# Kernel tuning notes

Measured on AMD Instinct MI355X. Metric: run time of the kernel, lower is better.

Reference implementation:

```python
import jax, jax.numpy as jnp
import numpy as np

B, H, W = 16, 512, 512


def conv2d(x, w, b):
    # NCHW conv, stride 1, padding 1 (SAME for 3x3)
    y = jax.lax.conv_general_dilated(
        x, w, window_strides=(1, 1), padding=((1, 1), (1, 1)),
        dimension_numbers=("NCHW", "OIHW", "NCHW"))
    return y + b[None, :, None, None]


def bilinear_sample(img, py, px):
    # img: [B,H,W]; py,px: [B,K,H,W] float sample coords. Zero padding outside.
    Hh, Ww = img.shape[1], img.shape[2]
    y0 = jnp.floor(py)
    x0 = jnp.floor(px)
    wy = py - y0  # fractional weights
    wx = px - x0
    y0i = y0.astype(jnp.int32)
    x0i = x0.astype(jnp.int32)

    def gather(yi, xi):
        valid = (yi >= 0) & (yi < Hh) & (xi >= 0) & (xi < Ww)
        yc = jnp.clip(yi, 0, Hh - 1)
        xc = jnp.clip(xi, 0, Ww - 1)
        v = jax.vmap(lambda im, yy, xx: im[yy, xx])(img, yc, xc)
        return jnp.where(valid, v, jnp.zeros((), img.dtype))

    v00 = gather(y0i, x0i)
    v01 = gather(y0i, x0i + 1)
    v10 = gather(y0i + 1, x0i)
    v11 = gather(y0i + 1, x0i + 1)
    return (v00 * (1 - wy) * (1 - wx) + v01 * (1 - wy) * wx
            + v10 * wy * (1 - wx) + v11 * wy * wx)


def setup_inputs() -> dict:
    key = jax.random.key(0)
    ks = jax.random.split(key, 7)
    pm25 = jax.random.normal(ks[0], (B, 1, H, W), jnp.float32)
    avg_wind = jax.random.normal(ks[1], (B, 2, H, W), jnp.float32)
    topo = jax.random.normal(ks[2], (B, 1, H, W), jnp.float32)
    # offset_conv params (Kaiming-ish small random)
    conv1_w = jax.random.normal(ks[3], (16, 3, 3, 3), jnp.float32) * (1.0 / np.sqrt(3 * 9))
    conv1_b = jax.random.normal(ks[4], (16,), jnp.float32) * 0.01
    conv2_w = jax.random.normal(ks[5], (18, 16, 3, 3), jnp.float32) * (1.0 / np.sqrt(16 * 9))
    conv2_b = jax.random.normal(ks[6], (18,), jnp.float32) * 0.01
    # dirac init: identity 3x3 kernel
    weight = jnp.zeros((1, 1, 3, 3), jnp.float32).at[0, 0, 1, 1].set(1.0)
    return {"pm25": pm25, "avg_wind": avg_wind, "topo": topo,
            "conv1_w": conv1_w, "conv1_b": conv1_b,
            "conv2_w": conv2_w, "conv2_b": conv2_b, "weight": weight}


def reference(pm25, avg_wind, topo, conv1_w, conv1_b, conv2_w, conv2_b, weight):
    # offset-predicting conv stack
    feat = jax.nn.gelu(conv2d(jnp.concatenate([avg_wind, topo], axis=1), conv1_w, conv1_b), approximate=False)
    offsets = conv2d(feat, conv2_w, conv2_b)          # [B, 2*3*3, H, W]
    b, _, h, w = offsets.shape
    off = offsets.reshape(b, 9, 2, h, w)              # k = i*3 + j; [.,k,0]=dy, [.,k,1]=dx
    dy, dx = off[:, :, 0], off[:, :, 1]               # [B,9,H,W]

    ys = jnp.arange(h, dtype=pm25.dtype)[None, None, :, None]
    xs = jnp.arange(w, dtype=pm25.dtype)[None, None, None, :]
    ki = jnp.arange(3, dtype=pm25.dtype)
    kdy = (jnp.repeat(ki, 3) - 1.0)[None, :, None, None]  # kernel row offset - pad
    kdx = (jnp.tile(ki, 3) - 1.0)[None, :, None, None]    # kernel col offset - pad

    py = ys + kdy + dy                                # sample rows   [B,9,H,W]
    px = xs + kdx + dx                                # sample cols   [B,9,H,W]

    samp = bilinear_sample(pm25[:, 0], py, px)        # [B,9,H,W]
    wk = weight.reshape(9)                            # single-channel 3x3 kernel
    out = jnp.einsum("bkhw,k->bhw", samp, wk)[:, None]
    return out                                        # [B,1,H,W]
```

## Files before the change

kernel.cpp:

```cpp
#include <hip/hip_runtime.h>
#include <math.h>

#define Bn 16
#define Hh 512
#define Ww 512
#define HW_ (Hh * Ww)
#define TILE 32
#define NTHREADS 1024
#define S 37
#define SIN_N 1400
#define NFP 1280
#define NT2 80

typedef __bf16 bfrag __attribute__((ext_vector_type(8)));
typedef __bf16 bf4   __attribute__((ext_vector_type(4)));
typedef float  ffrag __attribute__((ext_vector_type(16)));
typedef float  f32x4 __attribute__((ext_vector_type(4)));
typedef float  f32x2 __attribute__((ext_vector_type(2)));

__device__ __forceinline__ short f2bf(float f) {
    unsigned u = __float_as_uint(f);
    unsigned r = u + 0x7FFFu + ((u >> 16) & 1u);
    return (short)(r >> 16);
}

__device__ __forceinline__ f32x2 mk2(float a, float b) { f32x2 t; t.x = a; t.y = b; return t; }

__device__ __forceinline__ f32x2 gelu_fast2(f32x2 x) {
    f32x2 z = x * x;
    f32x2 a = z * 0.044715f + 1.0f;
    f32x2 u = (x * 2.302208199f) * a;
    f32x2 e;
    e.x = __builtin_amdgcn_exp2f(u.x);
    e.y = __builtin_amdgcn_exp2f(u.y);
    f32x2 r;
    r.x = __builtin_amdgcn_rcpf(e.x + 1.0f);
    r.y = __builtin_amdgcn_rcpf(e.y + 1.0f);
    return x - x * r;
}

__device__ __forceinline__ float bilin(const float* __restrict__ img, float py, float px) {
    float y0f = floorf(py), x0f = floorf(px);
    float wy = py - y0f, wx = px - x0f;
    int y0 = (int)y0f, x0 = (int)x0f;
    int yc0 = min(max(y0, 0), Hh - 1), yc1 = min(max(y0 + 1, 0), Hh - 1);
    int xc0 = min(max(x0, 0), Ww - 1), xc1 = min(max(x0 + 1, 0), Ww - 1);
    bool vy0 = (unsigned)y0 < (unsigned)Hh, vy1 = (unsigned)(y0 + 1) < (unsigned)Hh;
    bool vx0 = (unsigned)x0 < (unsigned)Ww, vx1 = (unsigned)(x0 + 1) < (unsigned)Ww;
    const float* r0 = img + yc0 * Ww;
    const float* r1 = img + yc1 * Ww;
    float v00 = (vy0 && vx0) ? r0[xc0] : 0.0f;
    float v01 = (vy0 && vx1) ? r0[xc1] : 0.0f;
    float v10 = (vy1 && vx0) ? r1[xc0] : 0.0f;
    float v11 = (vy1 && vx1) ? r1[xc1] : 0.0f;
    return (1.0f - wy) * ((1.0f - wx) * v00 + wx * v01) +
           wy          * ((1.0f - wx) * v10 + wx * v11);
}

__global__ void pack_w(const float* __restrict__ w2, const float* __restrict__ w1,
                       const float* __restrict__ b1, int* __restrict__ ws) {
    const int lane = threadIdx.x;
    const int l31  = lane & 31;
    const int lh   = lane >> 5;
    for (int tap = 0; tap < 9; ++tap) {
        int pk[4];
        #pragma unroll
        for (int jj = 0; jj < 4; ++jj) {
            float v0 = (l31 < 18) ? w2[(l31 * 16 + lh * 8 + 2 * jj    ) * 9 + tap] : 0.0f;
            float v1 = (l31 < 18) ? w2[(l31 * 16 + lh * 8 + 2 * jj + 1) * 9 + tap] : 0.0f;
            pk[jj] = ((int)(unsigned short)f2bf(v0)) | ((int)f2bf(v1) << 16);
        }
        ((int4*)ws)[tap * 64 + lane] = make_int4(pk[0], pk[1], pk[2], pk[3]);
    }
    const int m  = lane & 15;
    const int kq = lane >> 4;
    for (int t = 0; t < 2; ++t) {
        int pk[4];
        #pragma unroll
        for (int jj = 0; jj < 4; ++jj) {
            float vv[2];
            #pragma unroll
            for (int h = 0; h < 2; ++h) {
                int k   = kq * 8 + 2 * jj + h;
                int kyl = k >> 4, kx = (k >> 2) & 3, c = k & 3;
                int ky  = 2 * t + kyl;
                float x = 0.0f;
                if (kx < 3 && c < 3 && ky < 3) x = w1[m * 27 + c * 9 + ky * 3 + kx];
                if (t == 0 && k == 3) x = b1[m];
                vv[h] = x;
            }
            pk[jj] = ((int)(unsigned short)f2bf(vv[0])) | ((int)f2bf(vv[1]) << 16);
        }
        ((int4*)ws)[576 + t * 64 + lane] = make_int4(pk[0], pk[1], pk[2], pk[3]);
    }
}

#define SMEM_BYTES (SIN_N * 16 + 2 * NFP * 16)

__global__ __launch_bounds__(NTHREADS, 8) void residual_advection_fused(
    const float* __restrict__ pm25,
    const float* __restrict__ wind,
    const float* __restrict__ topo,
    const float* __restrict__ b2,
    const float* __restrict__ wt,
    const int*   __restrict__ wsB,
    float* __restrict__ out)
{
    __shared__ __align__(16) char smem[SMEM_BYTES];
    __bf16* s_in   = (__bf16*)smem;
    __bf16* s_feat = (__bf16*)(smem + SIN_N * 16);

    const int tid = threadIdx.x;
    const int bb  = blockIdx.z;
    const int ty0 = blockIdx.y * TILE;
    const int tx0 = blockIdx.x * TILE;
    const bool edge = (ty0 == 0) || (ty0 == Hh - TILE) || (tx0 == 0) || (tx0 == Ww - TILE);

    const int lane = tid & 63;
    const int wv   = tid >> 6;
    const int l31  = lane & 31;
    const int lh   = lane >> 5;

    const bfrag* WF = (const bfrag*)wsB;

    bfrag w1f0 = WF[576 + lane];
    bfrag w1f1 = WF[640 + lane];

    for (int idx = tid; idx < SIN_N; idx += NTHREADS) {
        float c0 = 0.0f, c1 = 0.0f, c2 = 0.0f;
        if (idx < 36 * S) {
            int r = idx / S, c = idx - r * S;
            int gy = ty0 - 2 + r, gx = tx0 - 2 + c;
            if ((unsigned)gy < (unsigned)Hh && (unsigned)gx < (unsigned)Ww) {
                int g = gy * Ww + gx;
                c0 = wind[(bb * 2 + 0) * HW_ + g];
                c1 = wind[(bb * 2 + 1) * HW_ + g];
                c2 = topo[bb * HW_ + g];
            }
        }
        bf4 v;
        v[0] = (__bf16)c0; v[1] = (__bf16)c1; v[2] = (__bf16)c2; v[3] = (__bf16)1.0f;
        *(bf4*)&s_in[idx * 8] = v;
        if (idx > 0) *(bf4*)&s_in[idx * 8 - 4] = v;
    }
    __syncthreads();

    {
        const int n    = lane & 15;
        const int kq   = lane >> 4;
        const int qoff = (kq >> 1) * S + (kq & 1) * 2;
        #pragma unroll
        for (int i = 0; i < 5; ++i) {
            const int p = (wv * 5 + i) * 16 + n;
            f32x4 acc;
            acc[0] = 0.0f; acc[1] = 0.0f; acc[2] = 0.0f; acc[3] = 0.0f;
            bfrag bx0 = *(const bfrag*)&s_in[(p + qoff) * 8];
            bfrag bx1 = *(const bfrag*)&s_in[(p + qoff + 2 * S) * 8];
            acc = __builtin_amdgcn_mfma_f32_16x16x32_bf16(w1f0, bx0, acc, 0, 0, 0);
            acc = __builtin_amdgcn_mfma_f32_16x16x32_bf16(w1f1, bx1, acc, 0, 0, 0);
            f32x2 g0 = gelu_fast2(mk2(acc[0], acc[1]));
            f32x2 g1 = gelu_fast2(mk2(acc[2], acc[3]));
            if (edge) {
                int fy = p / S;
                int fx = p - fy * S;
                int gy = ty0 + fy - 1, gx = tx0 + fx - 1;
                float msk = ((unsigned)gy < (unsigned)Hh && (unsigned)gx < (unsigned)Ww)
                            ? 1.0f : 0.0f;
                g0 *= msk; g1 *= msk;
            }
            bf4 w4;
            w4[0] = (__bf16)g0.x; w4[1] = (__bf16)g0.y;
            w4[2] = (__bf16)g1.x; w4[3] = (__bf16)g1.y;
            *(bf4*)&s_feat[((kq >> 1) * NFP + p) * 8 + (kq & 1) * 4] = w4;
        }
    }
    __syncthreads();

    ffrag a0, a1;
    #pragma unroll
    for (int r = 0; r < 16; ++r) { a0[r] = 0.0f; a1[r] = 0.0f; }
    {
        const int vb = (lh * NFP + (2 * wv) * S + l31) * 8;
        #pragma unroll
        for (int t = 0; t < 9; ++t) {
            const int toff = ((t / 3) * S + (t % 3)) * 8;
            bfrag wf = WF[t * 64 + lane];
            bfrag f0 = *(const bfrag*)&s_feat[vb + toff];
            bfrag f1 = *(const bfrag*)&s_feat[vb + toff + S * 8];
            a0 = __builtin_amdgcn_mfma_f32_32x32x16_bf16(wf, f0, a0, 0, 0, 0);
            a1 = __builtin_amdgcn_mfma_f32_32x32x16_bf16(wf, f1, a1, 0, 0, 0);
        }
    }

    {
        float ex[10];
        #pragma unroll
        for (int j = 0; j < 10; ++j) {
            float snd = lh ? a0[(j < 8) ? j : 7] : a1[j];
            ex[j] = __shfl_xor(snd, 32);
        }
        auto getv = [&](int row) -> float {
            if ((row & 4) == 0) {
                int r = (row < 8) ? row : ((row < 16) ? row - 4 : row - 8);
                return lh ? ex[r] : a0[r];
            } else {
                int r = (row & 3) + 4 * (row >> 3);
                return lh ? a1[r] : ex[r];
            }
        };
        const float* img = pm25 + bb * HW_;
        const int py_i = ty0 + 2 * wv + lh;
        const int px_i = tx0 + l31;
        const float fy = (float)py_i, fx = (float)px_i;
        float o = 0.0f;
        #pragma unroll
        for (int t = 0; t < 9; ++t) {
            float wk = wt[t];
            if (wk != 0.0f) {
                float dy = getv(2 * t)     + b2[2 * t];
                float dx = getv(2 * t + 1) + b2[2 * t + 1];
                float py = fy + (float)(t / 3 - 1) + dy;
                float px = fx + (float)(t % 3 - 1) + dx;
                o += wk * bilin(img, py, px);
            }
        }
        out[bb * HW_ + py_i * Ww + px_i] = o;
    }
}

extern "C" void kernel_launch(void* const* d_in, const int* in_sizes, int n_in,
                              void* d_out, int out_size, void* d_ws, size_t ws_size,
                              hipStream_t stream) {
    const float* pm25 = (const float*)d_in[0];
    const float* wind = (const float*)d_in[1];
    const float* topo = (const float*)d_in[2];
    const float* w1   = (const float*)d_in[3];
    const float* b1   = (const float*)d_in[4];
    const float* w2   = (const float*)d_in[5];
    const float* b2   = (const float*)d_in[6];
    const float* wt   = (const float*)d_in[7];
    float* o          = (float*)d_out;
    int*   wsB        = (int*)d_ws;

    pack_w<<<dim3(1), dim3(64), 0, stream>>>(w2, w1, b1, wsB);

    dim3 grid(Ww / TILE, Hh / TILE, Bn);
    residual_advection_fused<<<grid, dim3(NTHREADS), 0, stream>>>(
        pm25, wind, topo, b2, wt, wsB, o);
}
```

Before: 176.8 us.

## Use polynomial erf GELU, fast interior loads, regrouped MFMA loop, lazy shuffles

Replaces the exp/rcp tanh-style GELU with a clamped odd polynomial erf approximation. Adds a branch-free global load path for interior tiles, reorders the conv2 MFMA loop so each LDS feature fragment is loaded once and reused across kernel rows, and moves the cross-half lane shuffles into the sampling loop so only taps with nonzero weight pay for them. The polynomial GELU changes numerics slightly, and the reordering alters register pressure and instruction scheduling.

Result: no change. 176.8 us (-0.0%).

```diff
diff --git a/kernel.cpp b/kernel.cpp
--- a/kernel.cpp
+++ b/kernel.cpp
@@ -27,16 +27,20 @@
 __device__ __forceinline__ f32x2 mk2(float a, float b) { f32x2 t; t.x = a; t.y = b; return t; }
 
 __device__ __forceinline__ f32x2 gelu_fast2(f32x2 x) {
-    f32x2 z = x * x;
-    f32x2 a = z * 0.044715f + 1.0f;
-    f32x2 u = (x * 2.302208199f) * a;
-    f32x2 e;
-    e.x = __builtin_amdgcn_exp2f(u.x);
-    e.y = __builtin_amdgcn_exp2f(u.y);
-    f32x2 r;
-    r.x = __builtin_amdgcn_rcpf(e.x + 1.0f);
-    r.y = __builtin_amdgcn_rcpf(e.y + 1.0f);
-    return x - x * r;
+    const float C0 = 1.1259890f, C1 = -0.3565430f, C2 = 0.0848830f,
+                C3 = -0.0110610f, C4 = 0.0005820f;
+    f32x2 y = x * 0.70710678f;
+    f32x2 t;
+    t.x = fminf(fmaxf(y.x, -2.5f), 2.5f);
+    t.y = fminf(fmaxf(y.y, -2.5f), 2.5f);
+    f32x2 u = t * t;
+    f32x2 p = u * C4 + C3;
+    p = p * u + C2;
+    p = p * u + C1;
+    p = p * u + C0;
+    f32x2 e = t * p;
+    f32x2 h = x * 0.5f;
+    return h * e + h;
 }
 
 __device__ __forceinline__ float bilin(const float* __restrict__ img, float py, float px) {
@@ -130,12 +134,19 @@
         float c0 = 0.0f, c1 = 0.0f, c2 = 0.0f;
         if (idx < 36 * S) {
             int r = idx / S, c = idx - r * S;
-            int gy = ty0 - 2 + r, gx = tx0 - 2 + c;
-            if ((unsigned)gy < (unsigned)Hh && (unsigned)gx < (unsigned)Ww) {
-                int g = gy * Ww + gx;
+            if (!edge) {
+                int g = (ty0 - 2 + r) * Ww + (tx0 - 2 + c);
                 c0 = wind[(bb * 2 + 0) * HW_ + g];
                 c1 = wind[(bb * 2 + 1) * HW_ + g];
                 c2 = topo[bb * HW_ + g];
+            } else {
+                int gy = ty0 - 2 + r, gx = tx0 - 2 + c;
+                if ((unsigned)gy < (unsigned)Hh && (unsigned)gx < (unsigned)Ww) {
+                    int g = gy * Ww + gx;
+                    c0 = wind[(bb * 2 + 0) * HW_ + g];
+                    c1 = wind[(bb * 2 + 1) * HW_ + g];
+                    c2 = topo[bb * HW_ + g];
+                }
             }
         }
         bf4 v;
@@ -182,32 +193,24 @@
     {
         const int vb = (lh * NFP + (2 * wv) * S + l31) * 8;
         #pragma unroll
-        for (int t = 0; t < 9; ++t) {
-            const int toff = ((t / 3) * S + (t % 3)) * 8;
-            bfrag wf = WF[t * 64 + lane];
-            bfrag f0 = *(const bfrag*)&s_feat[vb + toff];
-            bfrag f1 = *(const bfrag*)&s_feat[vb + toff + S * 8];
-            a0 = __builtin_amdgcn_mfma_f32_32x32x16_bf16(wf, f0, a0, 0, 0, 0);
-            a1 = __builtin_amdgcn_mfma_f32_32x32x16_bf16(wf, f1, a1, 0, 0, 0);
+        for (int kx = 0; kx < 3; ++kx) {
+            bfrag f0 = *(const bfrag*)&s_feat[vb + (0 * S + kx) * 8];
+            bfrag f1 = *(const bfrag*)&s_feat[vb + (1 * S + kx) * 8];
+            bfrag f2 = *(const bfrag*)&s_feat[vb + (2 * S + kx) * 8];
+            bfrag f3 = *(const bfrag*)&s_feat[vb + (3 * S + kx) * 8];
+            bfrag w0 = WF[(0 * 3 + kx) * 64 + lane];
+            bfrag w1_ = WF[(1 * 3 + kx) * 64 + lane];
+            bfrag w2_ = WF[(2 * 3 + kx) * 64 + lane];
+            a0 = __builtin_amdgcn_mfma_f32_32x32x16_bf16(w0,  f0, a0, 0, 0, 0);
+            a1 = __builtin_amdgcn_mfma_f32_32x32x16_bf16(w0,  f1, a1, 0, 0, 0);
+            a0 = __builtin_amdgcn_mfma_f32_32x32x16_bf16(w1_, f1, a0, 0, 0, 0);
+            a1 = __builtin_amdgcn_mfma_f32_32x32x16_bf16(w1_, f2, a1, 0, 0, 0);
+            a0 = __builtin_amdgcn_mfma_f32_32x32x16_bf16(w2_, f2, a0, 0, 0, 0);
+            a1 = __builtin_amdgcn_mfma_f32_32x32x16_bf16(w2_, f3, a1, 0, 0, 0);
         }
     }
 
     {
-        float ex[10];
-        #pragma unroll
-        for (int j = 0; j < 10; ++j) {
-            float snd = lh ? a0[(j < 8) ? j : 7] : a1[j];
-            ex[j] = __shfl_xor(snd, 32);
-        }
-        auto getv = [&](int row) -> float {
-            if ((row & 4) == 0) {
-                int r = (row < 8) ? row : ((row < 16) ? row - 4 : row - 8);
-                return lh ? ex[r] : a0[r];
-            } else {
-                int r = (row & 3) + 4 * (row >> 3);
-                return lh ? a1[r] : ex[r];
-            }
-        };
         const float* img = pm25 + bb * HW_;
         const int py_i = ty0 + 2 * wv + lh;
         const int px_i = tx0 + l31;
@@ -217,8 +220,22 @@
         for (int t = 0; t < 9; ++t) {
             float wk = wt[t];
             if (wk != 0.0f) {
-                float dy = getv(2 * t)     + b2[2 * t];
-                float dx = getv(2 * t + 1) + b2[2 * t + 1];
+                const int o_h = (t >> 1) & 1;
+                const int rg  = ((2 * t) & 3) + 4 * (t >> 2);
+                float dy, dx;
+                if (o_h == 0) {
+                    float sy = __shfl_xor(a1[rg], 32);
+                    float sx = __shfl_xor(a1[rg + 1], 32);
+                    dy = lh ? sy : a0[rg];
+                    dx = lh ? sx : a0[rg + 1];
+                } else {
+                    float sy = __shfl_xor(a0[rg], 32);
+                    float sx = __shfl_xor(a0[rg + 1], 32);
+                    dy = lh ? a1[rg] : sy;
+                    dx = lh ? a1[rg + 1] : sx;
+                }
+                dy += b2[2 * t];
+                dx += b2[2 * t + 1];
                 float py = fy + (float)(t / 3 - 1) + dy;
                 float px = fx + (float)(t % 3 - 1) + dx;
                 o += wk * bilin(img, py, px);
```
